# Performance work log

Hardware: AMD Instinct MI355X
Metric: run time of the kernel (lower is better)

The kernel has to match this reference:

```python
import jax, jax.numpy as jnp
import numpy as np

VOCAB, EMB, HID, OUT = 50257, 512, 512, 2
B, T = 64, 1024

def setup_inputs() -> dict:
    key = jax.random.key(0)
    ks = jax.random.split(key, 8)
    s_e = 1.0 / np.sqrt(EMB)
    s_h = 1.0 / np.sqrt(HID)
    return {
        "x": jax.random.randint(ks[0], (B, T), 0, VOCAB, dtype=jnp.int64),
        "emb": jax.random.normal(ks[1], (VOCAB, EMB), jnp.float32) * 0.02,
        "w_ih": jax.random.uniform(ks[2], (4 * HID, EMB), jnp.float32, -s_h, s_h),
        "w_hh": jax.random.uniform(ks[3], (4 * HID, HID), jnp.float32, -s_h, s_h),
        "b_ih": jax.random.uniform(ks[4], (4 * HID,), jnp.float32, -s_h, s_h),
        "b_hh": jax.random.uniform(ks[5], (4 * HID,), jnp.float32, -s_h, s_h),
        "w_out": jax.random.uniform(ks[6], (OUT, HID), jnp.float32, -s_h, s_h),
        "b_out": jax.random.uniform(ks[7], (OUT,), jnp.float32, -s_h, s_h),
    }

def _lstm_last_hidden(e, w_ih, w_hh, b_ih, b_hh):
    # e: [B, T, E]. Precompute input projection for all timesteps (one big GEMM).
    Bc, Tc, _ = e.shape
    H = w_hh.shape[1]
    x_proj = jnp.einsum('bte,ge->btg', e, w_ih) + b_ih + b_hh  # [B, T, 4H]
    x_proj = jnp.transpose(x_proj, (1, 0, 2))                   # [T, B, 4H]

    def step(carry, xt):
        h, c = carry
        gates = xt + h @ w_hh.T                 # [B, 4H]
        i, f, g, o = jnp.split(gates, 4, axis=-1)  # PyTorch gate order i,f,g,o
        i = jax.nn.sigmoid(i)
        f = jax.nn.sigmoid(f)
        g = jnp.tanh(g)
        o = jax.nn.sigmoid(o)
        c = f * c + i * g
        h = o * jnp.tanh(c)
        return (h, c), None

    h0 = jnp.zeros((Bc, H), e.dtype)
    c0 = jnp.zeros((Bc, H), e.dtype)
    (h_last, _), _ = jax.lax.scan(step, (h0, c0), x_proj)
    return h_last  # [B, H] == output at last timestep

def reference(x, emb, w_ih, w_hh, b_ih, b_hh, w_out, b_out):
    e = emb[x]                                   # [B, T, E] embedding lookup
    h_last = _lstm_last_hidden(e, w_ih, w_hh, b_ih, b_hh)
    out = h_last @ w_out.T + b_out               # [B, OUT]
    return jnp.squeeze(out)
```

## Files before the change

### kernel.cpp

```cpp
#include <hip/hip_runtime.h>
#include <hip/hip_bf16.h>
#include <stdint.h>

typedef __bf16   bf16x8 __attribute__((ext_vector_type(8)));
typedef float    f32x4  __attribute__((ext_vector_type(4)));
typedef float    fl4    __attribute__((ext_vector_type(4)));
typedef uint32_t u32;
typedef unsigned long long u64;
typedef uint32_t u32x4  __attribute__((ext_vector_type(4)));

#define T_    1024
#define G4H   2048

__device__ __forceinline__ float bf2f(uint16_t b){
  u32 u = ((u32)b) << 16; float f; __builtin_memcpy(&f, &u, 4); return f;
}
__device__ __forceinline__ uint16_t f2bf(float f){
  u32 u; __builtin_memcpy(&u, &f, 4);
  u = u + 0x7fffu + ((u >> 16) & 1u);
  return (uint16_t)(u >> 16);
}
__device__ __forceinline__ float fsig(float x){ return 1.f / (1.f + __expf(-x)); }
__device__ __forceinline__ float ftanh(float x){
  float xc = fminf(fmaxf(x, -15.f), 15.f);
  float e  = __expf(2.f * xc);
  return (e - 1.f) / (e + 1.f);
}
__device__ __forceinline__ void gl_lds16(const void* g, void* l){
  __builtin_amdgcn_global_load_lds((const __attribute__((address_space(1))) void*)g,
                                   (__attribute__((address_space(3))) void*)l, 16, 0, 0);
}
__device__ __forceinline__ u32 umaxv(u32 a, u32 b){ return a > b ? a : b; }

__global__ void detect_i64(const u32* __restrict__ x, u32* __restrict__ flag){
  int gid = blockIdx.x * 256 + threadIdx.x;
  u32 v = x[1 + 2 * gid];
  if (v != 0u) atomicOr(flag, 1u);
}

__global__ __launch_bounds__(256) void gather_embed(
    const u32* __restrict__ x, const float* __restrict__ emb,
    uint16_t* __restrict__ e, const u32* __restrict__ flag){
  int row = blockIdx.x * 8 + (threadIdx.x >> 5);
  int c0  = (threadIdx.x & 31) * 16;
  u32 tok = (*flag != 0u) ? x[row] : x[2 * row];
  const float* s = emb + (size_t)tok * 512 + c0;
  fl4 a = *(const fl4*)(s);
  fl4 b = *(const fl4*)(s + 4);
  fl4 c = *(const fl4*)(s + 8);
  fl4 d = *(const fl4*)(s + 12);
  u32x4 q0 = { (u32)f2bf(a.x) | ((u32)f2bf(a.y) << 16),
               (u32)f2bf(a.z) | ((u32)f2bf(a.w) << 16),
               (u32)f2bf(b.x) | ((u32)f2bf(b.y) << 16),
               (u32)f2bf(b.z) | ((u32)f2bf(b.w) << 16) };
  u32x4 q1 = { (u32)f2bf(c.x) | ((u32)f2bf(c.y) << 16),
               (u32)f2bf(c.z) | ((u32)f2bf(c.w) << 16),
               (u32)f2bf(d.x) | ((u32)f2bf(d.y) << 16),
               (u32)f2bf(d.z) | ((u32)f2bf(d.w) << 16) };
  *(u32x4*)(e + (size_t)row * 512 + c0)     = q0;
  *(u32x4*)(e + (size_t)row * 512 + c0 + 8) = q1;
}

__global__ __launch_bounds__(256) void prep_w(
    const float* __restrict__ w_ih, const float* __restrict__ w_hh,
    const float* __restrict__ b_ih, const float* __restrict__ b_hh,
    uint16_t* __restrict__ wih, uint16_t* __restrict__ whi,
    uint16_t* __restrict__ wlo, float* __restrict__ bias){
  int bidx = blockIdx.x, t = threadIdx.x;
  if (bidx < 512){
    size_t i0 = (size_t)bidx * 2048 + t * 8;
    fl4 a = *(const fl4*)(w_ih + i0), b = *(const fl4*)(w_ih + i0 + 4);
    u32x4 q = { (u32)f2bf(a.x) | ((u32)f2bf(a.y) << 16),
                (u32)f2bf(a.z) | ((u32)f2bf(a.w) << 16),
                (u32)f2bf(b.x) | ((u32)f2bf(b.y) << 16),
                (u32)f2bf(b.z) | ((u32)f2bf(b.w) << 16) };
    *(u32x4*)(wih + i0) = q;
  } else if (bidx < 1024){
    size_t i0 = (size_t)(bidx - 512) * 2048 + t * 8;
    fl4 a = *(const fl4*)(w_hh + i0), b = *(const fl4*)(w_hh + i0 + 4);
    float v[8] = {a.x,a.y,a.z,a.w,b.x,b.y,b.z,b.w};
    uint16_t hi[8], lo[8];
    #pragma unroll
    for (int j = 0; j < 8; ++j){
      hi[j] = f2bf(v[j]);
      lo[j] = f2bf(v[j] - bf2f(hi[j]));
    }
    u32x4 qh = { (u32)hi[0]|((u32)hi[1]<<16), (u32)hi[2]|((u32)hi[3]<<16),
                 (u32)hi[4]|((u32)hi[5]<<16), (u32)hi[6]|((u32)hi[7]<<16) };
    u32x4 ql = { (u32)lo[0]|((u32)lo[1]<<16), (u32)lo[2]|((u32)lo[3]<<16),
                 (u32)lo[4]|((u32)lo[5]<<16), (u32)lo[6]|((u32)lo[7]<<16) };
    *(u32x4*)(whi + i0) = qh;
    *(u32x4*)(wlo + i0) = ql;
  } else {
    int i0 = t * 8;
    #pragma unroll
    for (int j = 0; j < 8; ++j) bias[i0 + j] = b_ih[i0 + j] + b_hh[i0 + j];
  }
}

__global__ __launch_bounds__(256,1) void gemm_xproj(
    const uint16_t* __restrict__ A, const uint16_t* __restrict__ Bw,
    uint16_t* __restrict__ C){
  __shared__ uint16_t As[128 * 64];
  __shared__ uint16_t Bs[128 * 64];
  int m0 = blockIdx.x * 128, n0 = blockIdx.y * 128;
  int tid = threadIdx.x, wid = tid >> 6, l = tid & 63;
  int wm = (wid >> 1) * 64, wn = (wid & 1) * 64;
  f32x4 zz = {0.f, 0.f, 0.f, 0.f};
  f32x4 acc[4][4];
  #pragma unroll
  for (int i = 0; i < 4; ++i)
    #pragma unroll
    for (int j = 0; j < 4; ++j) acc[i][j] = zz;
  const uint16_t* Ap = A  + (size_t)m0 * 512;
  const uint16_t* Bp = Bw + (size_t)n0 * 512;
  for (int kt = 0; kt < 8; ++kt){
    __syncthreads();
    #pragma unroll
    for (int i = 0; i < 4; ++i){
      int c = (i * 4 + wid) * 64 + l;
      int row = c >> 3, col = c & 7;
      int scol = col ^ (row & 7);
      gl_lds16(Ap + (size_t)row * 512 + kt * 64 + scol * 8, &As[c * 8]);
      gl_lds16(Bp + (size_t)row * 512 + kt * 64 + scol * 8, &Bs[c * 8]);
    }
    __syncthreads();
    #pragma unroll
    for (int kk = 0; kk < 2; ++kk){
      bf16x8 af[4], bfr[4];
      #pragma unroll
      for (int i = 0; i < 4; ++i){
        int ra = wm + i * 16 + (l & 15);
        int rb = wn + i * 16 + (l & 15);
        int ci = kk * 4 + (l >> 4);
        af[i]  = *(const bf16x8*)((const char*)As + (size_t)ra * 128 + ((ci ^ (ra & 7)) << 4));
        bfr[i] = *(const bf16x8*)((const char*)Bs + (size_t)rb * 128 + ((ci ^ (rb & 7)) << 4));
      }
      #pragma unroll
      for (int mi = 0; mi < 4; ++mi)
        #pragma unroll
        for (int ni = 0; ni < 4; ++ni)
          acc[mi][ni] = __builtin_amdgcn_mfma_f32_16x16x32_bf16(af[mi], bfr[ni], acc[mi][ni], 0, 0, 0);
    }
  }
  #pragma unroll
  for (int mi = 0; mi < 4; ++mi)
    #pragma unroll
    for (int ni = 0; ni < 4; ++ni)
      #pragma unroll
      for (int r = 0; r < 4; ++r){
        int m = m0 + wm + mi * 16 + (l >> 4) * 4 + r;
        int n = n0 + wn + ni * 16 + (l & 15);
        C[(size_t)m * 2048 + n] = f2bf(acc[mi][ni][r]);
      }
}

__global__ __launch_bounds__(256,1) void lstm_rec(
    const uint16_t* __restrict__ xp, const uint16_t* __restrict__ whi,
    const uint16_t* __restrict__ wlo, const float* __restrict__ bias,
    u32* __restrict__ hbuf, u32* __restrict__ flags){
  int bid = blockIdx.x;
  int g = bid & 3;
  int slice = bid >> 2;
  int tid = threadIdx.x, wid = tid >> 6, l = tid & 63;
  int n_local = wid * 16 + (l & 15);
  int u = slice * 16 + (n_local >> 2);
  int gate = n_local & 3;
  int grow = gate * 512 + u;
  int bquad = (l >> 4) * 4;

  bf16x8 Bhi[16], Blo[16];
  {
    const uint16_t* ph = whi + (size_t)grow * 512 + (l >> 4) * 8;
    const uint16_t* pl = wlo + (size_t)grow * 512 + (l >> 4) * 8;
    #pragma unroll
    for (int ks = 0; ks < 16; ++ks){
      Bhi[ks] = *(const bf16x8*)(ph + ks * 32);
      Blo[ks] = *(const bf16x8*)(pl + ks * 32);
    }
  }
  float biasr = bias[grow];
  float c_[4] = {0.f, 0.f, 0.f, 0.f};
  __shared__ uint16_t hhi[16 * 512];
  __shared__ uint16_t hlo[16 * 512];
  u32* hb0 = hbuf + (size_t)(g * 2 + 0) * (16 * 512);
  u32* hb1 = hbuf + (size_t)(g * 2 + 1) * (16 * 512);
  u32* flagg = flags + g * 128;
  const uint16_t* xpb = xp + (size_t)(g * 16 + bquad) * T_ * G4H + grow;
  int alive = 1000000;
  int pb_base = wid;
  int brow = l & 15;
  int rsig = (brow & 7) ^ ((brow >> 3) << 2);

  for (int t = 0; t < T_; ++t){
    uint16_t xpr[4];
    #pragma unroll
    for (int r = 0; r < 4; ++r)
      xpr[r] = xpb[(size_t)r * T_ * G4H + (size_t)t * G4H];
    if (t > 0){
      if (wid == 0){
        u64 fa = (u64)(uintptr_t)(flagg + l);
        for (;;){
          u32 f0, f1;
          asm volatile(
            "global_load_dword %0, %2, off sc0 sc1\n\t"
            "global_load_dword %1, %2, off offset:256 sc0 sc1\n\t"
            "s_waitcnt vmcnt(0)"
            : "=&v"(f0), "=&v"(f1) : "v"(fa) : "memory");
          if (__all(((int)(f0 - (u32)t) >= 0) && ((int)(f1 - (u32)t) >= 0))) break;
          if (--alive < 0) break;
        }
      }
    }
    __syncthreads();
    if (t > 0){
      const char* hb = (const char*)((t & 1) ? hb0 : hb1);
      u64 a0 = (u64)(uintptr_t)(hb + tid * 32);
      u64 a1 = a0 + 8192, a2 = a0 + 16384, a3 = a0 + 24576;
      u32 eoffc = (u32)(((t - 1) >> 1) & 1) << 30;
      u32x4 q0, q1, q2, q3, q4, q5, q6, q7;
      for (;;){
        asm volatile(
          "global_load_dwordx4 %0, %8, off sc0 sc1\n\t"
          "global_load_dwordx4 %1, %8, off offset:16 sc0 sc1\n\t"
          "global_load_dwordx4 %2, %9, off sc0 sc1\n\t"
          "global_load_dwordx4 %3, %9, off offset:16 sc0 sc1\n\t"
          "global_load_dwordx4 %4, %10, off sc0 sc1\n\t"
          "global_load_dwordx4 %5, %10, off offset:16 sc0 sc1\n\t"
          "global_load_dwordx4 %6, %11, off sc0 sc1\n\t"
          "global_load_dwordx4 %7, %11, off offset:16 sc0 sc1\n\t"
          "s_waitcnt vmcnt(0)"
          : "=&v"(q0), "=&v"(q1), "=&v"(q2), "=&v"(q3),
            "=&v"(q4), "=&v"(q5), "=&v"(q6), "=&v"(q7)
          : "v"(a0), "v"(a1), "v"(a2), "v"(a3) : "memory");
        u32 m = 0;
        #define VQ(Q) \
          m = umaxv(m, umaxv((Q.x - eoffc) & 0x7fffffffu, (Q.y - eoffc) & 0x7fffffffu)); \
          m = umaxv(m, umaxv((Q.z - eoffc) & 0x7fffffffu, (Q.w - eoffc) & 0x7fffffffu));
        VQ(q0) VQ(q1) VQ(q2) VQ(q3) VQ(q4) VQ(q5) VQ(q6) VQ(q7)
        #undef VQ
        if (m < 0x3f810000u) break;
        if (--alive < 0) break;
        __builtin_amdgcn_s_sleep(1);
      }
      u32 V[32];
      *(u32x4*)&V[0]  = q0; *(u32x4*)&V[4]  = q1;
      *(u32x4*)&V[8]  = q2; *(u32x4*)&V[12] = q3;
      *(u32x4*)&V[16] = q4; *(u32x4*)&V[20] = q5;
      *(u32x4*)&V[24] = q6; *(u32x4*)&V[28] = q7;
      #pragma unroll
      for (int j = 0; j < 4; ++j){
        int b = 4 * j + pb_base;
        int ssig = (b & 7) ^ ((b >> 3) << 2);
        int slot = l ^ ssig;
        u32 H[4], L[4];
        #pragma unroll
        for (int i = 0; i < 4; ++i){
          u32 a = V[8*j + 2*i]     - eoffc;
          u32 bb = V[8*j + 2*i + 1] - eoffc;
          H[i] = (a >> 16)     | (bb & 0xffff0000u);
          L[i] = (a & 0xffffu) | (bb << 16);
        }
        u32x4 qh = {H[0], H[1], H[2], H[3]};
        u32x4 ql = {L[0], L[1], L[2], L[3]};
        *(u32x4*)((char*)hhi + b * 1024 + slot * 16) = qh;
        *(u32x4*)((char*)hlo + b * 1024 + slot * 16) = ql;
      }
    }
    __syncthreads();
    f32x4 acc = {0.f, 0.f, 0.f, 0.f};
    if (t > 0){
      f32x4 accA = {0.f,0.f,0.f,0.f}, accB = accA, accC = accA;
      #pragma unroll
      for (int ks = 0; ks < 16; ++ks){
        int slot = (ks * 4 + (l >> 4)) ^ rsig;
        bf16x8 ah = *(const bf16x8*)((const char*)hhi + brow * 1024 + slot * 16);
        bf16x8 al = *(const bf16x8*)((const char*)hlo + brow * 1024 + slot * 16);
        accA = __builtin_amdgcn_mfma_f32_16x16x32_bf16(ah, Bhi[ks], accA, 0, 0, 0);
        accB = __builtin_amdgcn_mfma_f32_16x16x32_bf16(al, Bhi[ks], accB, 0, 0, 0);
        accC = __builtin_amdgcn_mfma_f32_16x16x32_bf16(ah, Blo[ks], accC, 0, 0, 0);
      }
      #pragma unroll
      for (int i = 0; i < 4; ++i) acc[i] = (accA[i] + accB[i]) + accC[i];
    }
    float hn[4];
    int qb = l & ~3;
    #pragma unroll
    for (int r = 0; r < 4; ++r){
      float pre = acc[r] + bf2f(xpr[r]) + biasr;
      float gi = __shfl(pre, qb + 0, 64);
      float gf = __shfl(pre, qb + 1, 64);
      float gg = __shfl(pre, qb + 2, 64);
      float go = __shfl(pre, qb + 3, 64);
      float i_ = fsig(gi), f_ = fsig(gf), g_ = ftanh(gg), o_ = fsig(go);
      c_[r] = f_ * c_[r] + i_ * g_;
      hn[r] = o_ * ftanh(c_[r]);
    }
    {
      int r = l & 3;
      u32 eoffp = (u32)((t >> 1) & 1) << 30;
      uint16_t hi = f2bf(hn[r]);
      uint16_t lo = f2bf(hn[r] - bf2f(hi));
      u32 packed = (((u32)hi << 16) | (u32)lo) + eoffp;
      u32* dst = ((t & 1) ? hb1 : hb0) + (size_t)(bquad + r) * 512 + u;
      __hip_atomic_store(dst, packed, __ATOMIC_RELAXED, __HIP_MEMORY_SCOPE_AGENT);
    }
    asm volatile("s_waitcnt vmcnt(0)" ::: "memory");
    if (l == 0)
      __hip_atomic_store(flagg + slice * 4 + wid, (u32)(t + 1),
                         __ATOMIC_RELAXED, __HIP_MEMORY_SCOPE_AGENT);
  }
}

__global__ void final_proj(const u32* __restrict__ hbuf, const float* __restrict__ w_out,
                           const float* __restrict__ b_out, float* __restrict__ out){
  int b = blockIdx.x;
  int g = b >> 4, bl = b & 15;
  const u32* hp = hbuf + (size_t)(g * 2 + 1) * (16 * 512) + bl * 512;
  int tid = threadIdx.x;
  float p0 = 0.f, p1 = 0.f;
  #pragma unroll
  for (int j = 0; j < 8; ++j){
    int k = tid * 8 + j;
    u32 pk = hp[k] - 0x40000000u;
    float h = bf2f((uint16_t)(pk >> 16)) + bf2f((uint16_t)(pk & 0xffffu));
    p0 += h * w_out[k];
    p1 += h * w_out[512 + k];
  }
  #pragma unroll
  for (int off = 32; off > 0; off >>= 1){
    p0 += __shfl_down(p0, off, 64);
    p1 += __shfl_down(p1, off, 64);
  }
  if (tid == 0){
    out[b * 2 + 0] = p0 + b_out[0];
    out[b * 2 + 1] = p1 + b_out[1];
  }
}

extern "C" void kernel_launch(void* const* d_in, const int* in_sizes, int n_in,
                              void* d_out, int out_size, void* d_ws, size_t ws_size,
                              hipStream_t stream){
  const u32*   x     = (const u32*)d_in[0];
  const float* emb   = (const float*)d_in[1];
  const float* w_ih  = (const float*)d_in[2];
  const float* w_hh  = (const float*)d_in[3];
  const float* b_ih  = (const float*)d_in[4];
  const float* b_hh  = (const float*)d_in[5];
  const float* w_out = (const float*)d_in[6];
  const float* b_out = (const float*)d_in[7];
  char* ws = (char*)d_ws;

  uint16_t* e     = (uint16_t*)(ws);
  uint16_t* xp    = (uint16_t*)(ws + 67108864ull);
  uint16_t* wih   = (uint16_t*)(ws + 335544320ull);
  uint16_t* whi   = (uint16_t*)(ws + 337641472ull);
  uint16_t* wlo   = (uint16_t*)(ws + 339738624ull);
  float*    bias  = (float*)   (ws + 341835776ull);
  u32*      flagw = (u32*)     (ws + 341843968ull);
  u32*      hbuf  = (u32*)     (ws + 341901312ull);
  u32*      flags = (u32*)     (ws + 342163456ull);

  hipMemsetAsync(flagw, 0, 4, stream);
  hipMemsetAsync(flags, 0, 4 * 128 * 4, stream);
  hipMemsetAsync(hbuf, 0xBF, 4ull * 8 * 16 * 512, stream);
  detect_i64  <<<128, 256, 0, stream>>>(x, flagw);
  gather_embed<<<8192, 256, 0, stream>>>(x, emb, e, flagw);
  prep_w      <<<1025, 256, 0, stream>>>(w_ih, w_hh, b_ih, b_hh, wih, whi, wlo, bias);
  gemm_xproj  <<<dim3(512, 16), 256, 0, stream>>>(e, wih, xp);
  lstm_rec    <<<128, 256, 0, stream>>>(xp, whi, wlo, bias, hbuf, flags);
  final_proj  <<<64, 64, 0, stream>>>(hbuf, w_out, b_out, (float*)d_out);
}
```

Before: 4.946 ms.

## Split batch into 8 groups and poll h-state directly via L2-coherent loads

The recurrent kernel now runs as 8 batch groups of 8 rows across 256 blocks instead of 4 groups of 16, which halves the per-block h exchange and doubles parallelism. The separate per-wave flag array is gone. Consumers poll the epoch-tagged h buffer itself with sc0 loads, first from an L2-scope copy, and fall back to a system-coherent copy with sleep if it does not converge. Producers write both copies. This is meant to cut the synchronisation latency on the critical path of each timestep, but it relies on L2 coherence across XCDs, and half of each MFMA's rows are wasted on zero padding.

```diff
diff --git a/kernel.cpp b/kernel.cpp
--- a/kernel.cpp
+++ b/kernel.cpp
@@ -31,6 +31,15 @@
                                    (__attribute__((address_space(3))) void*)l, 16, 0, 0);
 }
 __device__ __forceinline__ u32 umaxv(u32 a, u32 b){ return a > b ? a : b; }
+__device__ __forceinline__ u32 vmax16(u32x4 q0, u32x4 q1, u32x4 q2, u32x4 q3, u32 eoff){
+  u32 m = 0;
+  #define VQe(Q) \
+    m = umaxv(m, umaxv((Q.x - eoff) & 0x7fffffffu, (Q.y - eoff) & 0x7fffffffu)); \
+    m = umaxv(m, umaxv((Q.z - eoff) & 0x7fffffffu, (Q.w - eoff) & 0x7fffffffu));
+  VQe(q0) VQe(q1) VQe(q2) VQe(q3)
+  #undef VQe
+  return m;
+}
 
 __global__ void detect_i64(const u32* __restrict__ x, u32* __restrict__ flag){
   int gid = blockIdx.x * 256 + threadIdx.x;
@@ -158,16 +167,16 @@
 __global__ __launch_bounds__(256,1) void lstm_rec(
     const uint16_t* __restrict__ xp, const uint16_t* __restrict__ whi,
     const uint16_t* __restrict__ wlo, const float* __restrict__ bias,
-    u32* __restrict__ hbuf, u32* __restrict__ flags){
+    u32* __restrict__ hL2, u32* __restrict__ hIF){
   int bid = blockIdx.x;
-  int g = bid & 3;
-  int slice = bid >> 2;
+  int g = bid & 7;
+  int slice = bid >> 3;
   int tid = threadIdx.x, wid = tid >> 6, l = tid & 63;
   int n_local = wid * 16 + (l & 15);
   int u = slice * 16 + (n_local >> 2);
   int gate = n_local & 3;
   int grow = gate * 512 + u;
-  int bquad = (l >> 4) * 4;
+  int bq = ((l >> 4) & 1) * 4;
 
   bf16x8 Bhi[16], Blo[16];
   {
@@ -180,83 +189,87 @@
     }
   }
   float biasr = bias[grow];
-  float c_[4] = {0.f, 0.f, 0.f, 0.f};
+  float c0 = 0.f, c1 = 0.f, c2 = 0.f, c3 = 0.f;
   __shared__ uint16_t hhi[16 * 512];
   __shared__ uint16_t hlo[16 * 512];
-  u32* hb0 = hbuf + (size_t)(g * 2 + 0) * (16 * 512);
-  u32* hb1 = hbuf + (size_t)(g * 2 + 1) * (16 * 512);
-  u32* flagg = flags + g * 128;
-  const uint16_t* xpb = xp + (size_t)(g * 16 + bquad) * T_ * G4H + grow;
-  int alive = 1000000;
-  int pb_base = wid;
+  u32* L2b0 = hL2 + (size_t)g * 2 * 4096;
+  u32* L2b1 = L2b0 + 4096;
+  u32* IFb0 = hIF + (size_t)g * 2 * 4096;
+  u32* IFb1 = IFb0 + 4096;
+  const uint16_t* xpb = xp + (size_t)(g * 8 + bq) * T_ * G4H + grow;
+
+  {
+    u32x4 z = {0, 0, 0, 0};
+    #pragma unroll
+    for (int j = 0; j < 2; ++j){
+      int b2 = 8 + 4 * j + wid;
+      *(u32x4*)((char*)hhi + b2 * 1024 + l * 16) = z;
+      *(u32x4*)((char*)hlo + b2 * 1024 + l * 16) = z;
+    }
+  }
+  int mode = 0;
+  int alive = 2000000;
   int brow = l & 15;
   int rsig = (brow & 7) ^ ((brow >> 3) << 2);
 
   for (int t = 0; t < T_; ++t){
-    uint16_t xpr[4];
-    #pragma unroll
-    for (int r = 0; r < 4; ++r)
-      xpr[r] = xpb[(size_t)r * T_ * G4H + (size_t)t * G4H];
+    uint16_t xpr0 = xpb[(size_t)0 * T_ * G4H + (size_t)t * G4H];
+    uint16_t xpr1 = xpb[(size_t)1 * T_ * G4H + (size_t)t * G4H];
+    uint16_t xpr2 = xpb[(size_t)2 * T_ * G4H + (size_t)t * G4H];
+    uint16_t xpr3 = xpb[(size_t)3 * T_ * G4H + (size_t)t * G4H];
+    u32x4 q0, q1, q2, q3;
+    u32 eoffc = (t > 0) ? ((u32)(((t - 1) >> 1) & 1) << 30) : 0u;
     if (t > 0){
-      if (wid == 0){
-        u64 fa = (u64)(uintptr_t)(flagg + l);
+      const char* bL2 = (const char*)((t & 1) ? L2b0 : L2b1);
+      const char* bIF = (const char*)((t & 1) ? IFb0 : IFb1);
+      u64 a0 = (u64)(uintptr_t)bL2 + (u64)(tid * 32);
+      u64 a1 = a0 + 8192;
+      u64 f0 = (u64)(uintptr_t)bIF + (u64)(tid * 32);
+      u64 f1 = f0 + 8192;
+      bool ok = false;
+      if (mode == 0){
+        for (int it = 0; it < 1024; ++it){
+          asm volatile(
+            "global_load_dwordx4 %0, %4, off sc0\n\t"
+            "global_load_dwordx4 %1, %4, off offset:16 sc0\n\t"
+            "global_load_dwordx4 %2, %5, off sc0\n\t"
+            "global_load_dwordx4 %3, %5, off offset:16 sc0\n\t"
+            "s_waitcnt vmcnt(0)"
+            : "=&v"(q0), "=&v"(q1), "=&v"(q2), "=&v"(q3)
+            : "v"(a0), "v"(a1) : "memory");
+          if (vmax16(q0, q1, q2, q3, eoffc) < 0x3f810000u){ ok = true; break; }
+        }
+        if (!ok) mode = 1;
+      }
+      if (!ok){
         for (;;){
-          u32 f0, f1;
           asm volatile(
-            "global_load_dword %0, %2, off sc0 sc1\n\t"
-            "global_load_dword %1, %2, off offset:256 sc0 sc1\n\t"
+            "global_load_dwordx4 %0, %4, off sc0 sc1\n\t"
+            "global_load_dwordx4 %1, %4, off offset:16 sc0 sc1\n\t"
+            "global_load_dwordx4 %2, %5, off sc0 sc1\n\t"
+            "global_load_dwordx4 %3, %5, off offset:16 sc0 sc1\n\t"
             "s_waitcnt vmcnt(0)"
-            : "=&v"(f0), "=&v"(f1) : "v"(fa) : "memory");
-          if (__all(((int)(f0 - (u32)t) >= 0) && ((int)(f1 - (u32)t) >= 0))) break;
+            : "=&v"(q0), "=&v"(q1), "=&v"(q2), "=&v"(q3)
+            : "v"(f0), "v"(f1) : "memory");
+          if (vmax16(q0, q1, q2, q3, eoffc) < 0x3f810000u) break;
           if (--alive < 0) break;
+          __builtin_amdgcn_s_sleep(1);
         }
       }
     }
     __syncthreads();
     if (t > 0){
-      const char* hb = (const char*)((t & 1) ? hb0 : hb1);
-      u64 a0 = (u64)(uintptr_t)(hb + tid * 32);
-      u64 a1 = a0 + 8192, a2 = a0 + 16384, a3 = a0 + 24576;
-      u32 eoffc = (u32)(((t - 1) >> 1) & 1) << 30;
-      u32x4 q0, q1, q2, q3, q4, q5, q6, q7;
-      for (;;){
-        asm volatile(
-          "global_load_dwordx4 %0, %8, off sc0 sc1\n\t"
-          "global_load_dwordx4 %1, %8, off offset:16 sc0 sc1\n\t"
-          "global_load_dwordx4 %2, %9, off sc0 sc1\n\t"
-          "global_load_dwordx4 %3, %9, off offset:16 sc0 sc1\n\t"
-          "global_load_dwordx4 %4, %10, off sc0 sc1\n\t"
-          "global_load_dwordx4 %5, %10, off offset:16 sc0 sc1\n\t"
-          "global_load_dwordx4 %6, %11, off sc0 sc1\n\t"
-          "global_load_dwordx4 %7, %11, off offset:16 sc0 sc1\n\t"
-          "s_waitcnt vmcnt(0)"
-          : "=&v"(q0), "=&v"(q1), "=&v"(q2), "=&v"(q3),
-            "=&v"(q4), "=&v"(q5), "=&v"(q6), "=&v"(q7)
-          : "v"(a0), "v"(a1), "v"(a2), "v"(a3) : "memory");
-        u32 m = 0;
-        #define VQ(Q) \
-          m = umaxv(m, umaxv((Q.x - eoffc) & 0x7fffffffu, (Q.y - eoffc) & 0x7fffffffu)); \
-          m = umaxv(m, umaxv((Q.z - eoffc) & 0x7fffffffu, (Q.w - eoffc) & 0x7fffffffu));
-        VQ(q0) VQ(q1) VQ(q2) VQ(q3) VQ(q4) VQ(q5) VQ(q6) VQ(q7)
-        #undef VQ
-        if (m < 0x3f810000u) break;
-        if (--alive < 0) break;
-        __builtin_amdgcn_s_sleep(1);
-      }
-      u32 V[32];
+      u32 V[16];
       *(u32x4*)&V[0]  = q0; *(u32x4*)&V[4]  = q1;
       *(u32x4*)&V[8]  = q2; *(u32x4*)&V[12] = q3;
-      *(u32x4*)&V[16] = q4; *(u32x4*)&V[20] = q5;
-      *(u32x4*)&V[24] = q6; *(u32x4*)&V[28] = q7;
-      #pragma unroll
-      for (int j = 0; j < 4; ++j){
-        int b = 4 * j + pb_base;
-        int ssig = (b & 7) ^ ((b >> 3) << 2);
-        int slot = l ^ ssig;
+      #pragma unroll
+      for (int j = 0; j < 2; ++j){
+        int b = 4 * j + wid;
+        int slot = l ^ b;
         u32 H[4], L[4];
         #pragma unroll
         for (int i = 0; i < 4; ++i){
-          u32 a = V[8*j + 2*i]     - eoffc;
+          u32 a  = V[8*j + 2*i]     - eoffc;
           u32 bb = V[8*j + 2*i + 1] - eoffc;
           H[i] = (a >> 16)     | (bb & 0xffff0000u);
           L[i] = (a & 0xffffu) | (bb << 16);
@@ -270,53 +283,68 @@
     __syncthreads();
     f32x4 acc = {0.f, 0.f, 0.f, 0.f};
     if (t > 0){
-      f32x4 accA = {0.f,0.f,0.f,0.f}, accB = accA, accC = accA;
+      f32x4 aA = {0.f,0.f,0.f,0.f}, aB = aA, aC = aA;
       #pragma unroll
       for (int ks = 0; ks < 16; ++ks){
         int slot = (ks * 4 + (l >> 4)) ^ rsig;
         bf16x8 ah = *(const bf16x8*)((const char*)hhi + brow * 1024 + slot * 16);
         bf16x8 al = *(const bf16x8*)((const char*)hlo + brow * 1024 + slot * 16);
-        accA = __builtin_amdgcn_mfma_f32_16x16x32_bf16(ah, Bhi[ks], accA, 0, 0, 0);
-        accB = __builtin_amdgcn_mfma_f32_16x16x32_bf16(al, Bhi[ks], accB, 0, 0, 0);
-        accC = __builtin_amdgcn_mfma_f32_16x16x32_bf16(ah, Blo[ks], accC, 0, 0, 0);
-      }
-      #pragma unroll
-      for (int i = 0; i < 4; ++i) acc[i] = (accA[i] + accB[i]) + accC[i];
-    }
-    float hn[4];
+        aA = __builtin_amdgcn_mfma_f32_16x16x32_bf16(ah, Bhi[ks], aA, 0, 0, 0);
+        aB = __builtin_amdgcn_mfma_f32_16x16x32_bf16(al, Bhi[ks], aB, 0, 0, 0);
+        aC = __builtin_amdgcn_mfma_f32_16x16x32_bf16(ah, Blo[ks], aC, 0, 0, 0);
+      }
+      #pragma unroll
+      for (int i = 0; i < 4; ++i) acc[i] = (aA[i] + aB[i]) + aC[i];
+    }
+    float hn0, hn1, hn2, hn3;
     int qb = l & ~3;
-    #pragma unroll
-    for (int r = 0; r < 4; ++r){
-      float pre = acc[r] + bf2f(xpr[r]) + biasr;
-      float gi = __shfl(pre, qb + 0, 64);
-      float gf = __shfl(pre, qb + 1, 64);
-      float gg = __shfl(pre, qb + 2, 64);
-      float go = __shfl(pre, qb + 3, 64);
+    {
+      float pre = acc[0] + bf2f(xpr0) + biasr;
+      float gi = __shfl(pre, qb, 64), gf = __shfl(pre, qb + 1, 64);
+      float gg = __shfl(pre, qb + 2, 64), go = __shfl(pre, qb + 3, 64);
       float i_ = fsig(gi), f_ = fsig(gf), g_ = ftanh(gg), o_ = fsig(go);
-      c_[r] = f_ * c_[r] + i_ * g_;
-      hn[r] = o_ * ftanh(c_[r]);
+      c0 = f_ * c0 + i_ * g_; hn0 = o_ * ftanh(c0);
     }
     {
-      int r = l & 3;
-      u32 eoffp = (u32)((t >> 1) & 1) << 30;
-      uint16_t hi = f2bf(hn[r]);
-      uint16_t lo = f2bf(hn[r] - bf2f(hi));
-      u32 packed = (((u32)hi << 16) | (u32)lo) + eoffp;
-      u32* dst = ((t & 1) ? hb1 : hb0) + (size_t)(bquad + r) * 512 + u;
-      __hip_atomic_store(dst, packed, __ATOMIC_RELAXED, __HIP_MEMORY_SCOPE_AGENT);
-    }
-    asm volatile("s_waitcnt vmcnt(0)" ::: "memory");
-    if (l == 0)
-      __hip_atomic_store(flagg + slice * 4 + wid, (u32)(t + 1),
-                         __ATOMIC_RELAXED, __HIP_MEMORY_SCOPE_AGENT);
-  }
-}
-
-__global__ void final_proj(const u32* __restrict__ hbuf, const float* __restrict__ w_out,
+      float pre = acc[1] + bf2f(xpr1) + biasr;
+      float gi = __shfl(pre, qb, 64), gf = __shfl(pre, qb + 1, 64);
+      float gg = __shfl(pre, qb + 2, 64), go = __shfl(pre, qb + 3, 64);
+      float i_ = fsig(gi), f_ = fsig(gf), g_ = ftanh(gg), o_ = fsig(go);
+      c1 = f_ * c1 + i_ * g_; hn1 = o_ * ftanh(c1);
+    }
+    {
+      float pre = acc[2] + bf2f(xpr2) + biasr;
+      float gi = __shfl(pre, qb, 64), gf = __shfl(pre, qb + 1, 64);
+      float gg = __shfl(pre, qb + 2, 64), go = __shfl(pre, qb + 3, 64);
+      float i_ = fsig(gi), f_ = fsig(gf), g_ = ftanh(gg), o_ = fsig(go);
+      c2 = f_ * c2 + i_ * g_; hn2 = o_ * ftanh(c2);
+    }
+    {
+      float pre = acc[3] + bf2f(xpr3) + biasr;
+      float gi = __shfl(pre, qb, 64), gf = __shfl(pre, qb + 1, 64);
+      float gg = __shfl(pre, qb + 2, 64), go = __shfl(pre, qb + 3, 64);
+      float i_ = fsig(gi), f_ = fsig(gf), g_ = ftanh(gg), o_ = fsig(go);
+      c3 = f_ * c3 + i_ * g_; hn3 = o_ * ftanh(c3);
+    }
+    if (l < 32){
+      float hsel = (l & 2) ? ((l & 1) ? hn3 : hn2) : ((l & 1) ? hn1 : hn0);
+      uint16_t hi  = f2bf(hsel);
+      uint16_t lo2 = f2bf(hsel - bf2f(hi));
+      u32 packed = (((u32)hi << 16) | (u32)lo2) + ((u32)((t >> 1) & 1) << 30);
+      u32 idx = (u32)((bq + (l & 3)) * 512 + u);
+      u64 dL2 = (u64)(uintptr_t)(((t & 1) ? L2b1 : L2b0) + idx);
+      u64 dIF = (u64)(uintptr_t)(((t & 1) ? IFb1 : IFb0) + idx);
+      asm volatile("global_store_dword %0, %1, off sc0"     :: "v"(dL2), "v"(packed) : "memory");
+      asm volatile("global_store_dword %0, %1, off sc0 sc1" :: "v"(dIF), "v"(packed) : "memory");
+    }
+  }
+}
+
+__global__ void final_proj(const u32* __restrict__ hIF, const float* __restrict__ w_out,
                            const float* __restrict__ b_out, float* __restrict__ out){
   int b = blockIdx.x;
-  int g = b >> 4, bl = b & 15;
-  const u32* hp = hbuf + (size_t)(g * 2 + 1) * (16 * 512) + bl * 512;
+  int g = b >> 3, rb = b & 7;
+  const u32* hp = hIF + (size_t)(g * 2 + 1) * 4096 + rb * 512;
   int tid = threadIdx.x;
   float p0 = 0.f, p1 = 0.f;
   #pragma unroll
@@ -358,16 +386,16 @@
   uint16_t* wlo   = (uint16_t*)(ws + 339738624ull);
   float*    bias  = (float*)   (ws + 341835776ull);
   u32*      flagw = (u32*)     (ws + 341843968ull);
-  u32*      hbuf  = (u32*)     (ws + 341901312ull);
-  u32*      flags = (u32*)     (ws + 342163456ull);
+  u32*      hIF   = (u32*)     (ws + 341901312ull);
+  u32*      hL2   = (u32*)     (ws + 342163456ull);
 
   hipMemsetAsync(flagw, 0, 4, stream);
-  hipMemsetAsync(flags, 0, 4 * 128 * 4, stream);
-  hipMemsetAsync(hbuf, 0xBF, 4ull * 8 * 16 * 512, stream);
+  hipMemsetAsync(hIF, 0xBF, 8ull * 2 * 4096 * 4, stream);
+  hipMemsetAsync(hL2, 0xBF, 8ull * 2 * 4096 * 4, stream);
   detect_i64  <<<128, 256, 0, stream>>>(x, flagw);
   gather_embed<<<8192, 256, 0, stream>>>(x, emb, e, flagw);
   prep_w      <<<1025, 256, 0, stream>>>(w_ih, w_hh, b_ih, b_hh, wih, whi, wlo, bias);
   gemm_xproj  <<<dim3(512, 16), 256, 0, stream>>>(e, wih, xp);
-  lstm_rec    <<<128, 256, 0, stream>>>(xp, whi, wlo, bias, hbuf, flags);
-  final_proj  <<<64, 64, 0, stream>>>(hbuf, w_out, b_out, (float*)d_out);
-}
+  lstm_rec    <<<256, 256, 0, stream>>>(xp, whi, wlo, bias, hL2, hIF);
+  final_proj  <<<64, 64, 0, stream>>>(hIF, w_out, b_out, (float*)d_out);
+}
```

Result: slower. 12.26 ms (+147.9%).

## Interleave four batch groups per block and drop flag-based synchronization

Applied to the files above, without the earlier changes.

The recurrent kernel previously launched 128 blocks, one per (batch group, slice), and synchronized through per-step flag arrays plus polling of h buffers. It now launches 32 blocks, each handling all four 16-row batch groups in sequence within a timestep. Synchronization relies only on the epoch-tagged h values, so the flag stores, flag polling, flag memset and sleep are removed. The aim is to hide cross-block latency for one group behind compute on the others and to cut sync overhead. The trade-off is fewer active CUs and serialized per-group work inside each block.

```diff
diff --git a/kernel.cpp b/kernel.cpp
--- a/kernel.cpp
+++ b/kernel.cpp
@@ -31,6 +31,15 @@
                                    (__attribute__((address_space(3))) void*)l, 16, 0, 0);
 }
 __device__ __forceinline__ u32 umaxv(u32 a, u32 b){ return a > b ? a : b; }
+__device__ __forceinline__ u32 vmax16(u32x4 q0, u32x4 q1, u32x4 q2, u32x4 q3, u32 eoff){
+  u32 m = 0;
+  #define VQe(Q) \
+    m = umaxv(m, umaxv((Q.x - eoff) & 0x7fffffffu, (Q.y - eoff) & 0x7fffffffu)); \
+    m = umaxv(m, umaxv((Q.z - eoff) & 0x7fffffffu, (Q.w - eoff) & 0x7fffffffu));
+  VQe(q0) VQe(q1) VQe(q2) VQe(q3)
+  #undef VQe
+  return m;
+}
 
 __global__ void detect_i64(const u32* __restrict__ x, u32* __restrict__ flag){
   int gid = blockIdx.x * 256 + threadIdx.x;
@@ -158,10 +167,8 @@
 __global__ __launch_bounds__(256,1) void lstm_rec(
     const uint16_t* __restrict__ xp, const uint16_t* __restrict__ whi,
     const uint16_t* __restrict__ wlo, const float* __restrict__ bias,
-    u32* __restrict__ hbuf, u32* __restrict__ flags){
-  int bid = blockIdx.x;
-  int g = bid & 3;
-  int slice = bid >> 2;
+    u32* __restrict__ hbuf){
+  int slice = blockIdx.x;
   int tid = threadIdx.x, wid = tid >> 6, l = tid & 63;
   int n_local = wid * 16 + (l & 15);
   int u = slice * 16 + (n_local >> 2);
@@ -180,143 +187,129 @@
     }
   }
   float biasr = bias[grow];
-  float c_[4] = {0.f, 0.f, 0.f, 0.f};
+  float cst[4][4];
+  #pragma unroll
+  for (int s = 0; s < 4; ++s)
+    #pragma unroll
+    for (int r = 0; r < 4; ++r) cst[s][r] = 0.f;
   __shared__ uint16_t hhi[16 * 512];
   __shared__ uint16_t hlo[16 * 512];
-  u32* hb0 = hbuf + (size_t)(g * 2 + 0) * (16 * 512);
-  u32* hb1 = hbuf + (size_t)(g * 2 + 1) * (16 * 512);
-  u32* flagg = flags + g * 128;
-  const uint16_t* xpb = xp + (size_t)(g * 16 + bquad) * T_ * G4H + grow;
-  int alive = 1000000;
-  int pb_base = wid;
+  const uint16_t* xpb = xp + (size_t)bquad * (T_ * G4H) + grow;
+  int alive = 2000000;
   int brow = l & 15;
   int rsig = (brow & 7) ^ ((brow >> 3) << 2);
 
   for (int t = 0; t < T_; ++t){
-    uint16_t xpr[4];
-    #pragma unroll
-    for (int r = 0; r < 4; ++r)
-      xpr[r] = xpb[(size_t)r * T_ * G4H + (size_t)t * G4H];
-    if (t > 0){
-      if (wid == 0){
-        u64 fa = (u64)(uintptr_t)(flagg + l);
+    uint16_t xpr[4][4];
+    #pragma unroll
+    for (int s = 0; s < 4; ++s)
+      #pragma unroll
+      for (int r = 0; r < 4; ++r)
+        xpr[s][r] = xpb[(size_t)(16 * s + r) * (T_ * G4H) + (size_t)t * G4H];
+    u32 eoffc = (u32)(((t - 1) >> 1) & 1) << 30;
+    u32 eoffp = (u32)((t >> 1) & 1) << 30;
+
+    #pragma unroll
+    for (int s = 0; s < 4; ++s){
+      u32* sb0 = hbuf + (size_t)(s * 2 + 0) * 8192;
+      u32* sb1 = hbuf + (size_t)(s * 2 + 1) * 8192;
+      u32x4 q0, q1, q2, q3, q4, q5, q6, q7;
+      if (t > 0){
+        const char* hb = (const char*)((t & 1) ? sb0 : sb1);
+        u64 a0 = (u64)(uintptr_t)(hb + tid * 32);
+        u64 a1 = a0 + 8192, a2 = a0 + 16384, a3 = a0 + 24576;
         for (;;){
-          u32 f0, f1;
           asm volatile(
-            "global_load_dword %0, %2, off sc0 sc1\n\t"
-            "global_load_dword %1, %2, off offset:256 sc0 sc1\n\t"
+            "global_load_dwordx4 %0, %8, off sc0 sc1\n\t"
+            "global_load_dwordx4 %1, %8, off offset:16 sc0 sc1\n\t"
+            "global_load_dwordx4 %2, %9, off sc0 sc1\n\t"
+            "global_load_dwordx4 %3, %9, off offset:16 sc0 sc1\n\t"
+            "global_load_dwordx4 %4, %10, off sc0 sc1\n\t"
+            "global_load_dwordx4 %5, %10, off offset:16 sc0 sc1\n\t"
+            "global_load_dwordx4 %6, %11, off sc0 sc1\n\t"
+            "global_load_dwordx4 %7, %11, off offset:16 sc0 sc1\n\t"
             "s_waitcnt vmcnt(0)"
-            : "=&v"(f0), "=&v"(f1) : "v"(fa) : "memory");
-          if (__all(((int)(f0 - (u32)t) >= 0) && ((int)(f1 - (u32)t) >= 0))) break;
+            : "=&v"(q0), "=&v"(q1), "=&v"(q2), "=&v"(q3),
+              "=&v"(q4), "=&v"(q5), "=&v"(q6), "=&v"(q7)
+            : "v"(a0), "v"(a1), "v"(a2), "v"(a3) : "memory");
+          u32 m = umaxv(vmax16(q0, q1, q2, q3, eoffc), vmax16(q4, q5, q6, q7, eoffc));
+          if (m < 0x3f810000u) break;
           if (--alive < 0) break;
         }
       }
-    }
-    __syncthreads();
-    if (t > 0){
-      const char* hb = (const char*)((t & 1) ? hb0 : hb1);
-      u64 a0 = (u64)(uintptr_t)(hb + tid * 32);
-      u64 a1 = a0 + 8192, a2 = a0 + 16384, a3 = a0 + 24576;
-      u32 eoffc = (u32)(((t - 1) >> 1) & 1) << 30;
-      u32x4 q0, q1, q2, q3, q4, q5, q6, q7;
-      for (;;){
-        asm volatile(
-          "global_load_dwordx4 %0, %8, off sc0 sc1\n\t"
-          "global_load_dwordx4 %1, %8, off offset:16 sc0 sc1\n\t"
-          "global_load_dwordx4 %2, %9, off sc0 sc1\n\t"
-          "global_load_dwordx4 %3, %9, off offset:16 sc0 sc1\n\t"
-          "global_load_dwordx4 %4, %10, off sc0 sc1\n\t"
-          "global_load_dwordx4 %5, %10, off offset:16 sc0 sc1\n\t"
-          "global_load_dwordx4 %6, %11, off sc0 sc1\n\t"
-          "global_load_dwordx4 %7, %11, off offset:16 sc0 sc1\n\t"
-          "s_waitcnt vmcnt(0)"
-          : "=&v"(q0), "=&v"(q1), "=&v"(q2), "=&v"(q3),
-            "=&v"(q4), "=&v"(q5), "=&v"(q6), "=&v"(q7)
-          : "v"(a0), "v"(a1), "v"(a2), "v"(a3) : "memory");
-        u32 m = 0;
-        #define VQ(Q) \
-          m = umaxv(m, umaxv((Q.x - eoffc) & 0x7fffffffu, (Q.y - eoffc) & 0x7fffffffu)); \
-          m = umaxv(m, umaxv((Q.z - eoffc) & 0x7fffffffu, (Q.w - eoffc) & 0x7fffffffu));
-        VQ(q0) VQ(q1) VQ(q2) VQ(q3) VQ(q4) VQ(q5) VQ(q6) VQ(q7)
-        #undef VQ
-        if (m < 0x3f810000u) break;
-        if (--alive < 0) break;
-        __builtin_amdgcn_s_sleep(1);
-      }
-      u32 V[32];
-      *(u32x4*)&V[0]  = q0; *(u32x4*)&V[4]  = q1;
-      *(u32x4*)&V[8]  = q2; *(u32x4*)&V[12] = q3;
-      *(u32x4*)&V[16] = q4; *(u32x4*)&V[20] = q5;
-      *(u32x4*)&V[24] = q6; *(u32x4*)&V[28] = q7;
-      #pragma unroll
-      for (int j = 0; j < 4; ++j){
-        int b = 4 * j + pb_base;
-        int ssig = (b & 7) ^ ((b >> 3) << 2);
-        int slot = l ^ ssig;
-        u32 H[4], L[4];
+      __syncthreads();
+      if (t > 0){
+        u32 V[32];
+        *(u32x4*)&V[0]  = q0; *(u32x4*)&V[4]  = q1;
+        *(u32x4*)&V[8]  = q2; *(u32x4*)&V[12] = q3;
+        *(u32x4*)&V[16] = q4; *(u32x4*)&V[20] = q5;
+        *(u32x4*)&V[24] = q6; *(u32x4*)&V[28] = q7;
         #pragma unroll
-        for (int i = 0; i < 4; ++i){
-          u32 a = V[8*j + 2*i]     - eoffc;
-          u32 bb = V[8*j + 2*i + 1] - eoffc;
-          H[i] = (a >> 16)     | (bb & 0xffff0000u);
-          L[i] = (a & 0xffffu) | (bb << 16);
+        for (int j = 0; j < 4; ++j){
+          int b = 4 * j + wid;
+          int ssig = (b & 7) ^ ((b >> 3) << 2);
+          int slot = l ^ ssig;
+          u32 H[4], L[4];
+          #pragma unroll
+          for (int i = 0; i < 4; ++i){
+            u32 a  = V[8*j + 2*i]     - eoffc;
+            u32 bb = V[8*j + 2*i + 1] - eoffc;
+            H[i] = (a >> 16)     | (bb & 0xffff0000u);
+            L[i] = (a & 0xffffu) | (bb << 16);
+          }
+          u32x4 qh = {H[0], H[1], H[2], H[3]};
+          u32x4 ql = {L[0], L[1], L[2], L[3]};
+          *(u32x4*)((char*)hhi + b * 1024 + slot * 16) = qh;
+          *(u32x4*)((char*)hlo + b * 1024 + slot * 16) = ql;
         }
-        u32x4 qh = {H[0], H[1], H[2], H[3]};
-        u32x4 ql = {L[0], L[1], L[2], L[3]};
-        *(u32x4*)((char*)hhi + b * 1024 + slot * 16) = qh;
-        *(u32x4*)((char*)hlo + b * 1024 + slot * 16) = ql;
-      }
-    }
-    __syncthreads();
-    f32x4 acc = {0.f, 0.f, 0.f, 0.f};
-    if (t > 0){
-      f32x4 accA = {0.f,0.f,0.f,0.f}, accB = accA, accC = accA;
-      #pragma unroll
-      for (int ks = 0; ks < 16; ++ks){
-        int slot = (ks * 4 + (l >> 4)) ^ rsig;
-        bf16x8 ah = *(const bf16x8*)((const char*)hhi + brow * 1024 + slot * 16);
-        bf16x8 al = *(const bf16x8*)((const char*)hlo + brow * 1024 + slot * 16);
-        accA = __builtin_amdgcn_mfma_f32_16x16x32_bf16(ah, Bhi[ks], accA, 0, 0, 0);
-        accB = __builtin_amdgcn_mfma_f32_16x16x32_bf16(al, Bhi[ks], accB, 0, 0, 0);
-        accC = __builtin_amdgcn_mfma_f32_16x16x32_bf16(ah, Blo[ks], accC, 0, 0, 0);
-      }
-      #pragma unroll
-      for (int i = 0; i < 4; ++i) acc[i] = (accA[i] + accB[i]) + accC[i];
-    }
-    float hn[4];
-    int qb = l & ~3;
-    #pragma unroll
-    for (int r = 0; r < 4; ++r){
-      float pre = acc[r] + bf2f(xpr[r]) + biasr;
-      float gi = __shfl(pre, qb + 0, 64);
-      float gf = __shfl(pre, qb + 1, 64);
-      float gg = __shfl(pre, qb + 2, 64);
-      float go = __shfl(pre, qb + 3, 64);
-      float i_ = fsig(gi), f_ = fsig(gf), g_ = ftanh(gg), o_ = fsig(go);
-      c_[r] = f_ * c_[r] + i_ * g_;
-      hn[r] = o_ * ftanh(c_[r]);
-    }
-    {
-      int r = l & 3;
-      u32 eoffp = (u32)((t >> 1) & 1) << 30;
-      uint16_t hi = f2bf(hn[r]);
-      uint16_t lo = f2bf(hn[r] - bf2f(hi));
-      u32 packed = (((u32)hi << 16) | (u32)lo) + eoffp;
-      u32* dst = ((t & 1) ? hb1 : hb0) + (size_t)(bquad + r) * 512 + u;
-      __hip_atomic_store(dst, packed, __ATOMIC_RELAXED, __HIP_MEMORY_SCOPE_AGENT);
-    }
-    asm volatile("s_waitcnt vmcnt(0)" ::: "memory");
-    if (l == 0)
-      __hip_atomic_store(flagg + slice * 4 + wid, (u32)(t + 1),
-                         __ATOMIC_RELAXED, __HIP_MEMORY_SCOPE_AGENT);
+      }
+      __syncthreads();
+      f32x4 acc = {0.f, 0.f, 0.f, 0.f};
+      if (t > 0){
+        f32x4 aA = {0.f,0.f,0.f,0.f}, aB = aA, aC = aA;
+        #pragma unroll
+        for (int ks = 0; ks < 16; ++ks){
+          int slot = (ks * 4 + (l >> 4)) ^ rsig;
+          bf16x8 ah = *(const bf16x8*)((const char*)hhi + brow * 1024 + slot * 16);
+          bf16x8 al = *(const bf16x8*)((const char*)hlo + brow * 1024 + slot * 16);
+          aA = __builtin_amdgcn_mfma_f32_16x16x32_bf16(ah, Bhi[ks], aA, 0, 0, 0);
+          aB = __builtin_amdgcn_mfma_f32_16x16x32_bf16(al, Bhi[ks], aB, 0, 0, 0);
+          aC = __builtin_amdgcn_mfma_f32_16x16x32_bf16(ah, Blo[ks], aC, 0, 0, 0);
+        }
+        #pragma unroll
+        for (int i = 0; i < 4; ++i) acc[i] = (aA[i] + aB[i]) + aC[i];
+      }
+      float hn[4];
+      int qb = l & ~3;
+      #pragma unroll
+      for (int r = 0; r < 4; ++r){
+        float pre = acc[r] + bf2f(xpr[s][r]) + biasr;
+        float gi = __shfl(pre, qb + 0, 64);
+        float gf = __shfl(pre, qb + 1, 64);
+        float gg = __shfl(pre, qb + 2, 64);
+        float go = __shfl(pre, qb + 3, 64);
+        float i_ = fsig(gi), f_ = fsig(gf), g_ = ftanh(gg), o_ = fsig(go);
+        cst[s][r] = f_ * cst[s][r] + i_ * g_;
+        hn[r] = o_ * ftanh(cst[s][r]);
+      }
+      {
+        int r = l & 3;
+        float hsel = (l & 2) ? ((l & 1) ? hn[3] : hn[2]) : ((l & 1) ? hn[1] : hn[0]);
+        uint16_t hi  = f2bf(hsel);
+        uint16_t lo2 = f2bf(hsel - bf2f(hi));
+        u32 packed = (((u32)hi << 16) | (u32)lo2) + eoffp;
+        u32* dst = ((t & 1) ? sb1 : sb0) + (size_t)(bquad + r) * 512 + u;
+        __hip_atomic_store(dst, packed, __ATOMIC_RELAXED, __HIP_MEMORY_SCOPE_AGENT);
+      }
+    }
   }
 }
 
 __global__ void final_proj(const u32* __restrict__ hbuf, const float* __restrict__ w_out,
                            const float* __restrict__ b_out, float* __restrict__ out){
   int b = blockIdx.x;
-  int g = b >> 4, bl = b & 15;
-  const u32* hp = hbuf + (size_t)(g * 2 + 1) * (16 * 512) + bl * 512;
+  int s = b >> 4, rb = b & 15;
+  const u32* hp = hbuf + (size_t)(s * 2 + 1) * 8192 + rb * 512;
   int tid = threadIdx.x;
   float p0 = 0.f, p1 = 0.f;
   #pragma unroll
@@ -359,15 +352,13 @@
   float*    bias  = (float*)   (ws + 341835776ull);
   u32*      flagw = (u32*)     (ws + 341843968ull);
   u32*      hbuf  = (u32*)     (ws + 341901312ull);
-  u32*      flags = (u32*)     (ws + 342163456ull);
 
   hipMemsetAsync(flagw, 0, 4, stream);
-  hipMemsetAsync(flags, 0, 4 * 128 * 4, stream);
-  hipMemsetAsync(hbuf, 0xBF, 4ull * 8 * 16 * 512, stream);
+  hipMemsetAsync(hbuf, 0xBF, 4ull * 2 * 8192 * 4, stream);
   detect_i64  <<<128, 256, 0, stream>>>(x, flagw);
   gather_embed<<<8192, 256, 0, stream>>>(x, emb, e, flagw);
   prep_w      <<<1025, 256, 0, stream>>>(w_ih, w_hh, b_ih, b_hh, wih, whi, wlo, bias);
   gemm_xproj  <<<dim3(512, 16), 256, 0, stream>>>(e, wih, xp);
-  lstm_rec    <<<128, 256, 0, stream>>>(xp, whi, wlo, bias, hbuf, flags);
+  lstm_rec    <<<32, 256, 0, stream>>>(xp, whi, wlo, bias, hbuf);
   final_proj  <<<64, 64, 0, stream>>>(hbuf, w_out, b_out, (float*)d_out);
 }
```

Result: slower. 13.32 ms (+169.3%).
